# Optimization experiments

Measured on AMD Instinct MI355X. Metric: run time of the kernel, lower is better.

Reference implementation:

```python
import jax, jax.numpy as jnp
import numpy as np

B, S, H = 2, 1024, 768
D, HID = 24, 96            # hdim_proj_dim, hdim_mlp_hidden
VIN, VHID = 3 * H, 2 * max(128, H // 2)  # concat_hadam -> 3H; out_hid = 768
ALPHA0 = 0.05              # init_gate_hdim


def setup_inputs() -> dict:
    key = jax.random.key(0)
    ks = jax.random.split(key, 10)
    sc = 0.02
    return {
        "H_j": jax.random.normal(ks[0], (B, S, H), jnp.float32),
        "H_i": jax.random.normal(ks[1], (B, S, H), jnp.float32),
        "attn_mask": jnp.ones((B, S), jnp.float32),
        "Wpj": jax.random.normal(ks[2], (H, D), jnp.float32) * sc,
        "Wpi": jax.random.normal(ks[3], (H, D), jnp.float32) * sc,
        "W1": jax.random.normal(ks[4], (4 * D, HID), jnp.float32) * sc,
        "b1": jnp.zeros((HID,), jnp.float32),
        "W2": jax.random.normal(ks[5], (HID, 1), jnp.float32) * sc,
        "b2": jnp.zeros((1,), jnp.float32),
        "Wv1": jax.random.normal(ks[6], (VIN, VHID), jnp.float32) * sc,
        "bv1": jnp.zeros((VHID,), jnp.float32),
        "Wv2": jax.random.normal(ks[7], (VHID, H), jnp.float32) * sc,
        "bv2": jnp.zeros((H,), jnp.float32),
        "alpha": jnp.float32(ALPHA0),
    }


def reference(H_j, H_i, attn_mask, Wpj, Wpi, W1, b1, W2, b2, Wv1, bv1, Wv2, bv2, alpha):
    # token projections: [B,S,D]
    Zj = H_j @ Wpj
    Zi = H_i @ Wpi
    # 4-term pair MLP, decomposed so the [B,S,S,4D] concat is never built:
    # cat([Zj_pair, Zi_pair, Zj*Zi, |Zj-Zi|]) @ W1 == sum of 4 partial products
    W1a, W1b, W1c, W1d = W1[:D], W1[D:2 * D], W1[2 * D:3 * D], W1[3 * D:]
    tj = Zj @ W1a                                   # [B,S,HID]
    ti = Zi @ W1b                                   # [B,S,HID]
    had = jnp.einsum('bsd,btd,dh->bsth', Zj, Zi, W1c)          # [B,S,S,HID]
    diff = jnp.abs(Zj[:, :, None, :] - Zi[:, None, :, :]) @ W1d  # [B,S,S,HID]
    h = jax.nn.relu(tj[:, :, None, :] + ti[:, None, :, :] + had + diff + b1)
    logits = (h @ W2)[..., 0] + b2[0]               # [B,S,S]
    # additive mask on key axis (torch: (1-mask)*finfo.min)
    logits = logits + (1.0 - attn_mask[:, None, :]) * jnp.finfo(logits.dtype).min
    probs = jax.nn.softmax(logits, axis=-1)
    ctx = jnp.einsum('bst,bth->bsh', probs, H_i)    # context over H_i
    # value fusion: concat_hadam -> [ctx, H_j, ctx*H_j]
    msg_in = jnp.concatenate([ctx, H_j, ctx * H_j], axis=-1)
    msg = jax.nn.relu(msg_in @ Wv1 + bv1) @ Wv2 + bv2
    return alpha * msg  # dropout is identity at eval
```

## Files before the change

### kernel.cpp

```cpp
#include <hip/hip_runtime.h>
#include <math.h>

#define BB   2
#define SS   1024
#define HH   768
#define DD   24
#define HIDD 96
#define VINN 2304
#define VHIDD 768
#define NRR  2048

typedef __attribute__((ext_vector_type(8))) short short8;
typedef __attribute__((ext_vector_type(4))) float floatx4;

static __device__ inline unsigned short f2bf(float x) {
    unsigned int u = __float_as_uint(x);
    u = (u + 0x7FFFu + ((u >> 16) & 1u)) >> 16;
    return (unsigned short)u;
}
static __device__ inline unsigned int pack2(float a, float b) {
    return (unsigned int)f2bf(a) | ((unsigned int)f2bf(b) << 16);
}

static __device__ inline void gl16(const unsigned short* g, unsigned short* l) {
    __builtin_amdgcn_global_load_lds(
        (const __attribute__((address_space(1))) unsigned int*)g,
        (__attribute__((address_space(3))) unsigned int*)l,
        16, 0, 0);
}

__global__ __launch_bounds__(256) void k_zproj(
    const float* __restrict__ Hj, const float* __restrict__ Hi,
    const float* __restrict__ Wpj, const float* __restrict__ Wpi,
    unsigned* __restrict__ Zjp, unsigned* __restrict__ Zip)
{
    __shared__ __align__(16) unsigned short sAz[64][72];
    __shared__ __align__(16) unsigned short sBTz[32][72];
    int tid = threadIdx.x;
    int w = tid >> 6, lane = tid & 63;
    int quad = lane >> 4, col = lane & 15;
    int m0 = blockIdx.x * 64;
    bool isJ = (m0 < NRR);
    const float* src = isJ ? Hj : Hi;
    const float* Wp  = isJ ? Wpj : Wpi;
    unsigned* Zp     = isJ ? Zjp : Zip;
    int rowbase = isJ ? m0 : (m0 - NRR);

    floatx4 acc[2];
    acc[0] = (floatx4){0.f,0.f,0.f,0.f};
    acc[1] = (floatx4){0.f,0.f,0.f,0.f};

    for (int kb = 0; kb < HH; kb += 64) {
        #pragma unroll
        for (int i = 0; i < 4; ++i) {
            int f4 = tid + i*256;
            int r = f4 >> 4, c4 = f4 & 15;
            float4 v = *(const float4*)(src + (size_t)(rowbase + r)*HH + kb + c4*4);
            uint2 pkt; pkt.x = pack2(v.x, v.y); pkt.y = pack2(v.z, v.w);
            *(uint2*)&sAz[r][c4*4] = pkt;
        }
        {
            const float* wsrc = Wp + (size_t)kb*DD;
            #pragma unroll
            for (int i = 0; i < 6; ++i) {
                int idx = tid + i*256;
                int k = idx / DD, n = idx % DD;
                sBTz[n][k] = f2bf(wsrc[idx]);
            }
        }
        __syncthreads();
        #pragma unroll
        for (int kt = 0; kt < 2; ++kt) {
            short8 av = *(const short8*)&sAz[w*16 + col][kt*32 + quad*8];
            #pragma unroll
            for (int nt = 0; nt < 2; ++nt) {
                short8 bv = *(const short8*)&sBTz[nt*16 + col][kt*32 + quad*8];
                acc[nt] = __builtin_amdgcn_mfma_f32_16x16x32_bf16(av, bv, acc[nt], 0, 0, 0);
            }
        }
        __syncthreads();
    }
    #pragma unroll
    for (int nt = 0; nt < 2; ++nt) {
        #pragma unroll
        for (int r = 0; r < 4; ++r) {
            float v = acc[nt][r];
            float vn = __shfl_xor(v, 1, 64);
            int n = nt*16 + col;
            if (!(col & 1) && n < DD) {
                int m = w*16 + quad*4 + r;
                Zp[(size_t)(rowbase + m)*12 + (n >> 1)] = pack2(v, vn);
            }
        }
    }
}

#define LSTR 72
#define TC 64
__global__ __launch_bounds__(256) void k_attn(
    const unsigned* __restrict__ Zjp, const unsigned* __restrict__ Zip,
    const float* __restrict__ W1, const float* __restrict__ b1,
    const float* __restrict__ W2,
    const float* __restrict__ mask, unsigned short* __restrict__ probs,
    const float* __restrict__ Hi, const float* __restrict__ Wv1,
    const float* __restrict__ Wv2,
    unsigned short* __restrict__ Wv1T, unsigned short* __restrict__ Wv2T,
    unsigned short* __restrict__ HiT)
{
    int tid = threadIdx.x;
    __shared__ __align__(16) unsigned short sAB[2][TC*LSTR];
    __shared__ __align__(16) float sLog[SS];
    __shared__ unsigned sZjp[12];
    __shared__ float sW2[HIDD];
    __shared__ float sRed[4];
    unsigned short* sABf = &sAB[0][0];

    if (blockIdx.x >= NRR) {
        int b2 = blockIdx.x - NRR;
        const float* in; unsigned short* out; int R, C, r0, c0;
        if (b2 < 1728) {
            in = Wv1; out = Wv1T; R = VINN; C = VHIDD;
            c0 = (b2 % 24) * 32; r0 = (b2 / 24) * 32;
        } else if (b2 < 2304) {
            int t = b2 - 1728;
            in = Wv2; out = Wv2T; R = VHIDD; C = HH;
            c0 = (t % 24) * 32; r0 = (t / 24) * 32;
        } else {
            int t = b2 - 2304;
            int z = t / 768; t %= 768;
            in = Hi + (size_t)z*SS*HH; out = HiT + (size_t)z*HH*SS;
            R = SS; C = HH;
            c0 = (t % 24) * 32; r0 = (t / 24) * 32;
        }
        float* tile = (float*)sABf;
        int tc = tid & 31, tr = tid >> 5;
        #pragma unroll
        for (int i = 0; i < 4; ++i)
            tile[(tr + i*8)*33 + tc] = in[(size_t)(r0 + tr + i*8)*C + c0 + tc];
        __syncthreads();
        #pragma unroll
        for (int i = 0; i < 4; ++i)
            out[(size_t)(c0 + tr + i*8)*R + r0 + tc] = f2bf(tile[tc*33 + tr + i*8]);
        return;
    }

    int row = blockIdx.x;
    int b = row >> 10;
    int lane = tid & 63, wv = tid >> 6;
    int quad = lane >> 4, col = lane & 15;

    if (tid < 12) sZjp[tid] = Zjp[(size_t)row*12 + tid];
    if (tid < HIDD) sW2[tid] = W2[tid];
    __syncthreads();

    if (tid < HIDD) {
        int h = tid;
        float zj[24];
        #pragma unroll
        for (int u = 0; u < 12; ++u) {
            unsigned z = sZjp[u];
            zj[2*u]   = __uint_as_float(z << 16);
            zj[2*u+1] = __uint_as_float(z & 0xffff0000u);
        }
        float tj = b1[h];
        #pragma unroll
        for (int d = 0; d < DD; ++d) tj = fmaf(zj[d], W1[d*HIDD + h], tj);
        unsigned short* rowp = sABf + h*LSTR;
        #pragma unroll
        for (int d = 0; d < DD; ++d)
            rowp[d] = f2bf(fmaf(zj[d], W1[(48+d)*HIDD + h], W1[(24+d)*HIDD + h]));
        #pragma unroll
        for (int d = 0; d < DD; ++d)
            rowp[24+d] = f2bf(W1[(72+d)*HIDD + h]);
        rowp[48] = f2bf(tj);
        #pragma unroll
        for (int k = 49; k < 64; ++k) rowp[k] = 0;
    }
    __syncthreads();

    short8 bfr[6][2];
    #pragma unroll
    for (int nf = 0; nf < 6; ++nf)
        #pragma unroll
        for (int kt = 0; kt < 2; ++kt)
            bfr[nf][kt] = *(const short8*)&sABf[(nf*16 + col)*LSTR + kt*32 + quad*8];
    float4 w2q[6];
    #pragma unroll
    for (int nf = 0; nf < 6; ++nf)
        w2q[nf] = *(const float4*)&sW2[nf*16 + quad*4];
    __syncthreads();

    if (tid < 128) {
        int bf = tid >> 6, r = tid & 63;
        unsigned short* rowp = &sAB[bf][r*LSTR];
        uint4 w0; w0.x = 0x3F80u; w0.y = 0; w0.z = 0; w0.w = 0;
        *(uint4*)&rowp[48] = w0;
        uint4 zz; zz.x = 0; zz.y = 0; zz.z = 0; zz.w = 0;
        *(uint4*)&rowp[56] = zz;
    }

    int t_loc = tid >> 2, ss = tid & 3;
    const unsigned* zbase = Zip + (size_t)(b << 10) * 12;

    float zalo[3], zahi[3];
    #pragma unroll
    for (int u = 0; u < 3; ++u) {
        unsigned za = sZjp[3*ss + u];
        zalo[u] = __uint_as_float(za << 16);
        zahi[u] = __uint_as_float(za & 0xffff0000u);
    }

    auto pack = [&](int chunk, int bf) {
        int t = chunk*TC + t_loc;
        const unsigned* zr = zbase + (size_t)t*12;
        unsigned short* rowp = &sAB[bf][t_loc*LSTR];
        if (ss < 3) {
            uint4 cp = *(const uint4*)(zr + 4*ss);
            *(uint4*)&rowp[8*ss] = cp;
        }
        unsigned myz[3];
        #pragma unroll
        for (int u = 0; u < 3; ++u) myz[u] = zr[3*ss + u];
        #pragma unroll
        for (int u = 0; u < 3; ++u) {
            unsigned zb = myz[u];
            float blo = __uint_as_float(zb << 16);
            float bhi = __uint_as_float(zb & 0xffff0000u);
            unsigned dlo = __float_as_uint(fabsf(zalo[u] - blo)) + 0x8000u;
            unsigned dhi = __float_as_uint(fabsf(zahi[u] - bhi)) + 0x8000u;
            *(unsigned*)&rowp[24 + 6*ss + 2*u] =
                __builtin_amdgcn_perm(dhi, dlo, 0x07060302u);
        }
    };

    pack(0, 0);
    __syncthreads();

    for (int chunk = 0; chunk < SS/TC; ++chunk) {
        int cur = chunk & 1;
        if (chunk + 1 < SS/TC) pack(chunk + 1, cur ^ 1);

        int arow = wv*16 + col;
        short8 av0 = *(const short8*)&sAB[cur][arow*LSTR + quad*8];
        short8 av1 = *(const short8*)&sAB[cur][arow*LSTR + 32 + quad*8];
        float s0 = 0.f;
        #pragma unroll
        for (int hf = 0; hf < 6; ++hf) {
            floatx4 a0 = {0.f,0.f,0.f,0.f};
            a0 = __builtin_amdgcn_mfma_f32_16x16x32_bf16(bfr[hf][0], av0, a0, 0, 0, 0);
            a0 = __builtin_amdgcn_mfma_f32_16x16x32_bf16(bfr[hf][1], av1, a0, 0, 0, 0);
            float w2v[4] = {w2q[hf].x, w2q[hf].y, w2q[hf].z, w2q[hf].w};
            #pragma unroll
            for (int r = 0; r < 4; ++r)
                s0 = fmaf(fmaxf(a0[r], 0.f), w2v[r], s0);
        }
        s0 += __shfl_xor(s0, 16, 64);
        s0 += __shfl_xor(s0, 32, 64);
        if (lane < 16)
            sLog[chunk*TC + wv*16 + lane] = s0;
        __syncthreads();
    }

    float lv[4];
    #pragma unroll
    for (int i = 0; i < 4; ++i) {
        int t = tid + i*256;
        lv[i] = sLog[t] + (1.0f - mask[(size_t)(b<<10) + t]) * (-3.402823466e+38f);
    }
    float m = fmaxf(fmaxf(lv[0], lv[1]), fmaxf(lv[2], lv[3]));
    #pragma unroll
    for (int off = 32; off; off >>= 1) m = fmaxf(m, __shfl_down(m, off, 64));
    if (lane == 0) sRed[wv] = m;
    __syncthreads();
    float M = fmaxf(fmaxf(sRed[0], sRed[1]), fmaxf(sRed[2], sRed[3]));
    float e[4]; float ssum = 0.f;
    #pragma unroll
    for (int i = 0; i < 4; ++i) { e[i] = expf(lv[i] - M); ssum += e[i]; }
    #pragma unroll
    for (int off = 32; off; off >>= 1) ssum += __shfl_down(ssum, off, 64);
    __syncthreads();
    if (lane == 0) sRed[wv] = ssum;
    __syncthreads();
    float inv = 1.0f / (sRed[0] + sRed[1] + sRed[2] + sRed[3]);
    #pragma unroll
    for (int i = 0; i < 4; ++i)
        probs[(size_t)row*SS + tid + i*256] = f2bf(e[i] * inv);
}

template<int MODE>
__global__ __launch_bounds__(256) void k_mgemm_nf(
    const unsigned short* __restrict__ A,
    const unsigned short* __restrict__ BT,
    const float* __restrict__ bias,
    const float* __restrict__ Hj,
    const float* __restrict__ alpha_p,
    void* __restrict__ Cout,
    int K, int bt_bstride)
{
    __shared__ __align__(16) unsigned short sA[64*64];
    __shared__ __align__(16) unsigned short sB[32*64];
    int tid = threadIdx.x;
    int w = tid >> 6, lane = tid & 63;
    int quad = lane >> 4, col = lane & 15;

    int n0 = blockIdx.x * 32, m0 = blockIdx.y * 64;
    int nk = K >> 6;
    const unsigned short* Bb = BT + (size_t)(m0 >> 10) * bt_bstride;

    int srow = lane >> 3;
    int skc  = (lane & 7) * 8;

    floatx4 acc[2];
    acc[0] = (floatx4){0.f,0.f,0.f,0.f};
    acc[1] = (floatx4){0.f,0.f,0.f,0.f};

    for (int kb = 0; kb < nk; ++kb) {
        int kofs = kb*64;
        gl16(A  + (size_t)(m0 + w*16     + srow)*K + kofs + skc, &sA[(w*16)*64]);
        gl16(A  + (size_t)(m0 + w*16 + 8 + srow)*K + kofs + skc, &sA[(w*16 + 8)*64]);
        gl16(Bb + (size_t)(n0 + w*8      + srow)*K + kofs + skc, &sB[(w*8)*64]);
        __syncthreads();
        #pragma unroll
        for (int kt = 0; kt < 2; ++kt) {
            short8 av = *(const short8*)&sA[(w*16 + col)*64 + kt*32 + quad*8];
            #pragma unroll
            for (int nf = 0; nf < 2; ++nf) {
                short8 bv = *(const short8*)&sB[(nf*16 + col)*64 + kt*32 + quad*8];
                acc[nf] = __builtin_amdgcn_mfma_f32_16x16x32_bf16(av, bv, acc[nf], 0, 0, 0);
            }
        }
        __syncthreads();
    }

    float alpha = (MODE == 2) ? alpha_p[0] : 1.0f;
    #pragma unroll
    for (int nf = 0; nf < 2; ++nf) {
        int n = n0 + nf*16 + col;
        #pragma unroll
        for (int r = 0; r < 4; ++r) {
            int m = w*16 + quad*4 + r;
            size_t g = (size_t)(m0 + m);
            float v = acc[nf][r];
            if (MODE == 0) {
                float hj = Hj[g*HH + n];
                unsigned short* msgin = (unsigned short*)Cout;
                msgin[g*VINN + n]        = f2bf(v);
                msgin[g*VINN + HH + n]   = f2bf(hj);
                msgin[g*VINN + 2*HH + n] = f2bf(v*hj);
            } else if (MODE == 1) {
                ((unsigned short*)Cout)[g*VHIDD + n] =
                    f2bf(fmaxf(v + bias[n], 0.f));
            } else {
                ((float*)Cout)[g*HH + n] = alpha*(v + bias[n]);
            }
        }
    }
}

extern "C" void kernel_launch(void* const* d_in, const int* in_sizes, int n_in,
                              void* d_out, int out_size, void* d_ws, size_t ws_size,
                              hipStream_t stream)
{
    const float* Hj   = (const float*)d_in[0];
    const float* Hi   = (const float*)d_in[1];
    const float* mask = (const float*)d_in[2];
    const float* Wpj  = (const float*)d_in[3];
    const float* Wpi  = (const float*)d_in[4];
    const float* W1   = (const float*)d_in[5];
    const float* b1   = (const float*)d_in[6];
    const float* W2   = (const float*)d_in[7];
    const float* Wv1  = (const float*)d_in[9];
    const float* bv1  = (const float*)d_in[10];
    const float* Wv2  = (const float*)d_in[11];
    const float* bv2  = (const float*)d_in[12];
    const float* alpha = (const float*)d_in[13];
    float* out = (float*)d_out;

    const int NR = NRR;
    char* p = (char*)d_ws;
    auto alloc = [&](size_t bytes) {
        char* r = p; p += (bytes + 255) & ~(size_t)255; return r;
    };
    unsigned* Zjp          = (unsigned*)alloc((size_t)NR*12*4);
    unsigned* Zip          = (unsigned*)alloc((size_t)NR*12*4);
    unsigned short* probsb = (unsigned short*)alloc((size_t)NR*SS*2);
    unsigned short* HiT    = (unsigned short*)alloc((size_t)BB*HH*SS*2);
    unsigned short* Wv1T   = (unsigned short*)alloc((size_t)VHIDD*VINN*2);
    unsigned short* Wv2T   = (unsigned short*)alloc((size_t)HH*VHIDD*2);
    unsigned short* msginb = (unsigned short*)alloc((size_t)NR*VINN*2);
    unsigned short* Y1b    = (unsigned short*)alloc((size_t)NR*VHIDD*2);

    k_zproj<<<2*NR/64, 256, 0, stream>>>(Hj, Hi, Wpj, Wpi, Zjp, Zip);

    k_attn<<<NR + 1728 + 576 + 1536, 256, 0, stream>>>(
        Zjp, Zip, W1, b1, W2, mask, probsb,
        Hi, Wv1, Wv2, Wv1T, Wv2T, HiT);

    k_mgemm_nf<0><<<dim3(HH/32, NR/64), 256, 0, stream>>>(
        probsb, HiT, nullptr, Hj, alpha, msginb, SS, HH*SS);

    k_mgemm_nf<1><<<dim3(VHIDD/32, NR/64), 256, 0, stream>>>(
        msginb, Wv1T, bv1, nullptr, alpha, Y1b, VINN, 0);

    k_mgemm_nf<2><<<dim3(HH/32, NR/64), 256, 0, stream>>>(
        Y1b, Wv2T, bv2, nullptr, alpha, out, VHIDD, 0);
}
```

Measured before the change: 198.7 us.

## Widen attention block to 512 threads and pipeline Zi loads through registers

```diff
diff --git a/kernel.cpp b/kernel.cpp
--- a/kernel.cpp
+++ b/kernel.cpp
@@ -19,7 +19,9 @@
     return (unsigned short)u;
 }
 static __device__ inline unsigned int pack2(float a, float b) {
-    return (unsigned int)f2bf(a) | ((unsigned int)f2bf(b) << 16);
+    unsigned int r;
+    asm("v_cvt_pk_bf16_f32 %0, %1, %2" : "=v"(r) : "v"(a), "v"(b));
+    return r;
 }
 
 static __device__ inline void gl16(const unsigned short* g, unsigned short* l) {
@@ -96,8 +98,9 @@
 }
 
 #define LSTR 72
-#define TC 64
-__global__ __launch_bounds__(256) void k_attn(
+#define TC 128
+#define NC (SS/TC)
+__global__ __launch_bounds__(512, 4) void k_attn(
     const unsigned* __restrict__ Zjp, const unsigned* __restrict__ Zip,
     const float* __restrict__ W1, const float* __restrict__ b1,
     const float* __restrict__ W2,
@@ -112,7 +115,7 @@
     __shared__ __align__(16) float sLog[SS];
     __shared__ unsigned sZjp[12];
     __shared__ float sW2[HIDD];
-    __shared__ float sRed[4];
+    __shared__ float sRed[8];
     unsigned short* sABf = &sAB[0][0];
 
     if (blockIdx.x >= NRR) {
@@ -135,12 +138,12 @@
         float* tile = (float*)sABf;
         int tc = tid & 31, tr = tid >> 5;
         #pragma unroll
-        for (int i = 0; i < 4; ++i)
-            tile[(tr + i*8)*33 + tc] = in[(size_t)(r0 + tr + i*8)*C + c0 + tc];
-        __syncthreads();
-        #pragma unroll
-        for (int i = 0; i < 4; ++i)
-            out[(size_t)(c0 + tr + i*8)*R + r0 + tc] = f2bf(tile[tc*33 + tr + i*8]);
+        for (int i = 0; i < 2; ++i)
+            tile[(tr + i*16)*33 + tc] = in[(size_t)(r0 + tr + i*16)*C + c0 + tc];
+        __syncthreads();
+        #pragma unroll
+        for (int i = 0; i < 2; ++i)
+            out[(size_t)(c0 + tr + i*16)*R + r0 + tc] = f2bf(tile[tc*33 + tr + i*16]);
         return;
     }
 
@@ -190,8 +193,8 @@
         w2q[nf] = *(const float4*)&sW2[nf*16 + quad*4];
     __syncthreads();
 
-    if (tid < 128) {
-        int bf = tid >> 6, r = tid & 63;
+    if (tid < 256) {
+        int bf = tid >> 7, r = tid & 127;
         unsigned short* rowp = &sAB[bf][r*LSTR];
         uint4 w0; w0.x = 0x3F80u; w0.y = 0; w0.z = 0; w0.w = 0;
         *(uint4*)&rowp[48] = w0;
@@ -210,40 +213,32 @@
         zahi[u] = __uint_as_float(za & 0xffff0000u);
     }
 
-    auto pack = [&](int chunk, int bf) {
+    auto issue = [&](int chunk, uint4 &cp, unsigned (&mz)[3]) {
         int t = chunk*TC + t_loc;
         const unsigned* zr = zbase + (size_t)t*12;
+        if (ss < 3) cp = *(const uint4*)(zr + 4*ss);
+        #pragma unroll
+        for (int u = 0; u < 3; ++u) mz[u] = zr[3*ss + u];
+    };
+    auto packw = [&](int bf, const uint4 &cp, const unsigned (&mz)[3]) {
         unsigned short* rowp = &sAB[bf][t_loc*LSTR];
-        if (ss < 3) {
-            uint4 cp = *(const uint4*)(zr + 4*ss);
-            *(uint4*)&rowp[8*ss] = cp;
-        }
-        unsigned myz[3];
-        #pragma unroll
-        for (int u = 0; u < 3; ++u) myz[u] = zr[3*ss + u];
+        if (ss < 3) *(uint4*)&rowp[8*ss] = cp;
         #pragma unroll
         for (int u = 0; u < 3; ++u) {
-            unsigned zb = myz[u];
+            unsigned zb = mz[u];
             float blo = __uint_as_float(zb << 16);
             float bhi = __uint_as_float(zb & 0xffff0000u);
-            unsigned dlo = __float_as_uint(fabsf(zalo[u] - blo)) + 0x8000u;
-            unsigned dhi = __float_as_uint(fabsf(zahi[u] - bhi)) + 0x8000u;
-            *(unsigned*)&rowp[24 + 6*ss + 2*u] =
-                __builtin_amdgcn_perm(dhi, dlo, 0x07060302u);
+            float dlo = fabsf(zalo[u] - blo);
+            float dhi = fabsf(zahi[u] - bhi);
+            *(unsigned*)&rowp[24 + 6*ss + 2*u] = pack2(dlo, dhi);
         }
     };
-
-    pack(0, 0);
-    __syncthreads();
-
-    for (int chunk = 0; chunk < SS/TC; ++chunk) {
-        int cur = chunk & 1;
-        if (chunk + 1 < SS/TC) pack(chunk + 1, cur ^ 1);
-
+    auto mfma_fold = [&](int chunk, int cur) {
         int arow = wv*16 + col;
         short8 av0 = *(const short8*)&sAB[cur][arow*LSTR + quad*8];
         short8 av1 = *(const short8*)&sAB[cur][arow*LSTR + 32 + quad*8];
         float s0 = 0.f;
+        __builtin_amdgcn_s_setprio(1);
         #pragma unroll
         for (int hf = 0; hf < 6; ++hf) {
             floatx4 a0 = {0.f,0.f,0.f,0.f};
@@ -254,37 +249,60 @@
             for (int r = 0; r < 4; ++r)
                 s0 = fmaf(fmaxf(a0[r], 0.f), w2v[r], s0);
         }
+        __builtin_amdgcn_s_setprio(0);
         s0 += __shfl_xor(s0, 16, 64);
         s0 += __shfl_xor(s0, 32, 64);
         if (lane < 16)
             sLog[chunk*TC + wv*16 + lane] = s0;
-        __syncthreads();
-    }
-
-    float lv[4];
-    #pragma unroll
-    for (int i = 0; i < 4; ++i) {
-        int t = tid + i*256;
+    };
+
+    uint4 cpA, cpB; unsigned mzA[3], mzB[3];
+    issue(0, cpA, mzA);
+    issue(1, cpB, mzB);
+    packw(0, cpA, mzA);
+    __syncthreads();
+
+    #pragma unroll
+    for (int cc = 0; cc < NC; cc += 2) {
+        if (cc + 2 < NC) issue(cc + 2, cpA, mzA);
+        mfma_fold(cc, 0);
+        packw(1, cpB, mzB);
+        __syncthreads();
+        if (cc + 3 < NC) issue(cc + 3, cpB, mzB);
+        mfma_fold(cc + 1, 1);
+        if (cc + 2 < NC) packw(0, cpA, mzA);
+        __syncthreads();
+    }
+
+    float lv[2];
+    #pragma unroll
+    for (int i = 0; i < 2; ++i) {
+        int t = tid + i*512;
         lv[i] = sLog[t] + (1.0f - mask[(size_t)(b<<10) + t]) * (-3.402823466e+38f);
     }
-    float m = fmaxf(fmaxf(lv[0], lv[1]), fmaxf(lv[2], lv[3]));
+    float m = fmaxf(lv[0], lv[1]);
     #pragma unroll
     for (int off = 32; off; off >>= 1) m = fmaxf(m, __shfl_down(m, off, 64));
     if (lane == 0) sRed[wv] = m;
     __syncthreads();
-    float M = fmaxf(fmaxf(sRed[0], sRed[1]), fmaxf(sRed[2], sRed[3]));
-    float e[4]; float ssum = 0.f;
-    #pragma unroll
-    for (int i = 0; i < 4; ++i) { e[i] = expf(lv[i] - M); ssum += e[i]; }
+    float M = sRed[0];
+    #pragma unroll
+    for (int j = 1; j < 8; ++j) M = fmaxf(M, sRed[j]);
+    float e[2]; float ssum = 0.f;
+    #pragma unroll
+    for (int i = 0; i < 2; ++i) { e[i] = expf(lv[i] - M); ssum += e[i]; }
     #pragma unroll
     for (int off = 32; off; off >>= 1) ssum += __shfl_down(ssum, off, 64);
     __syncthreads();
     if (lane == 0) sRed[wv] = ssum;
     __syncthreads();
-    float inv = 1.0f / (sRed[0] + sRed[1] + sRed[2] + sRed[3]);
-    #pragma unroll
-    for (int i = 0; i < 4; ++i)
-        probs[(size_t)row*SS + tid + i*256] = f2bf(e[i] * inv);
+    float sum = sRed[0];
+    #pragma unroll
+    for (int j = 1; j < 8; ++j) sum += sRed[j];
+    float inv = 1.0f / sum;
+    #pragma unroll
+    for (int i = 0; i < 2; ++i)
+        probs[(size_t)row*SS + tid + i*512] = f2bf(e[i] * inv);
 }
 
 template<int MODE>
@@ -392,7 +410,7 @@
 
     k_zproj<<<2*NR/64, 256, 0, stream>>>(Hj, Hi, Wpj, Wpi, Zjp, Zip);
 
-    k_attn<<<NR + 1728 + 576 + 1536, 256, 0, stream>>>(
+    k_attn<<<NR + 1728 + 576 + 1536, 512, 0, stream>>>(
         Zjp, Zip, W1, b1, W2, mask, probsb,
         Hi, Wv1, Wv2, Wv1T, Wv2T, HiT);
 
```

Result: no change. 198.6 us (-0.1%).
